# Performance work log

Hardware: AMD Instinct MI355X
Metric: run time of the kernel (lower is better)

The kernel has to match this reference:

```python
import jax, jax.numpy as jnp
import numpy as np

B, T, D, H = 512, 1024, 12, 100


def setup_inputs() -> dict:
    key = jax.random.key(0)
    ks = jax.random.split(key, 5)
    x = jax.random.normal(ks[0], (B, T, D), dtype=jnp.float32)
    Wx = jax.random.normal(ks[1], (D, 4 * H), dtype=jnp.float32) * (1.0 / np.sqrt(D))
    Wh = jax.random.normal(ks[2], (H, 4 * H), dtype=jnp.float32) * (1.0 / np.sqrt(H))
    b = jnp.zeros((4 * H,), dtype=jnp.float32)
    Wd = jax.random.normal(ks[3], (H, D), dtype=jnp.float32) * (1.0 / np.sqrt(H))
    bd = jnp.zeros((D,), dtype=jnp.float32)
    return {"x": x, "Wx": Wx, "Wh": Wh, "b": b, "Wd": Wd, "bd": bd}


def _lstm_seq(x, Wx, Wh, b):
    # Precompute input projection for all timesteps (vectorized GEMM).
    xg = jnp.einsum('btd,dh->bth', x, Wx) + b  # [B, T, 4H]
    xg = jnp.transpose(xg, (1, 0, 2))          # [T, B, 4H] for scan

    def step(carry, xg_t):
        h, c = carry
        z = xg_t + h @ Wh                      # [B, 4H]
        i, f, g, o = jnp.split(z, 4, axis=-1)  # Keras gate order: i, f, c, o
        i = jax.nn.sigmoid(i)
        f = jax.nn.sigmoid(f)
        g = jnp.tanh(g)
        o = jax.nn.sigmoid(o)
        c = f * c + i * g
        h = o * jnp.tanh(c)
        return (h, c), h

    h0 = jnp.zeros((x.shape[0], Wh.shape[0]), dtype=x.dtype)
    c0 = jnp.zeros_like(h0)
    _, hs = jax.lax.scan(step, (h0, c0), xg)   # hs: [T, B, H]
    return jnp.transpose(hs, (1, 0, 2))        # [B, T, H]


def reference(x, Wx, Wh, b, Wd, bd):
    hs = _lstm_seq(x, Wx, Wh, b)               # [B, T, H]
    return jnp.einsum('bth,hd->btd', hs, Wd) + bd  # [B, T, 12]
```

## Files before the change

kernel.cpp:

```cpp
#include <hip/hip_runtime.h>
#include <math.h>

#define T_LEN 1024
#define BATCH 512
#define DIN   12
#define HID   100
#define G4    400
#define MB    4
#define NBLK  (BATCH / MB)
#define AROW  160
#define NW    8
#define NTHR  (NW * 64)
#define CHUNK 64
#define UNROLL 8

typedef _Float16 half8   __attribute__((ext_vector_type(8)));
typedef _Float16 half4_t __attribute__((ext_vector_type(4)));
typedef float    f32x4   __attribute__((ext_vector_type(4)));

static __device__ __forceinline__ float fast_exp2(float v) {
#if __has_builtin(__builtin_amdgcn_exp2f)
    return __builtin_amdgcn_exp2f(v);
#else
    return exp2f(v);
#endif
}
static __device__ __forceinline__ float fast_rcp(float v) {
#if __has_builtin(__builtin_amdgcn_rcpf)
    return __builtin_amdgcn_rcpf(v);
#else
    return 1.0f / v;
#endif
}

__launch_bounds__(NTHR, 2)
__global__ void lstm_mfma_kernel(const float* __restrict__ x,
                                 const float* __restrict__ Wx,
                                 const float* __restrict__ Wh,
                                 const float* __restrict__ b,
                                 const float* __restrict__ Wd,
                                 const float* __restrict__ bd,
                                 float* __restrict__ out) {
    __shared__ __align__(16) char smem[65536];
    const int tid  = threadIdx.x;
    const int wid  = tid >> 6;
    const int lane = tid & 63;
    const int l    = lane & 15;
    const int quad = lane >> 4;
    const int b0   = blockIdx.x * MB;
    const int j    = wid * 16 + l;

    _Float16* stage = (_Float16*)smem;
    half8 bfrag[4][4];
#pragma unroll
    for (int pass = 0; pass < 2; ++pass) {
#pragma unroll
        for (int gg = 0; gg < 2; ++gg) {
            const int G = pass * 2 + gg;
#pragma unroll
            for (int kt = 0; kt < 4; ++kt) {
                half8 v;
#pragma unroll
                for (int jj = 0; jj < 8; ++jj) {
                    const int k = kt * 32 + quad * 8 + jj;
                    float w = 0.f;
                    if (wid < 7) {
                        if (j < HID) {
                            if (k < HID)            w = Wh[k * G4 + G * HID + j];
                            else if (k < HID + DIN) w = Wx[(k - HID) * G4 + G * HID + j];
                        }
                    } else if (G == 0) {
                        if (l < DIN && k < HID)     w = Wd[k * DIN + l];
                    }
                    v[jj] = (_Float16)w;
                }
                *(half8*)&stage[((wid * 8) + (gg * 4 + kt)) * 512 + lane * 8] = v;
            }
        }
        __syncthreads();
#pragma unroll
        for (int gg = 0; gg < 2; ++gg)
#pragma unroll
            for (int kt = 0; kt < 4; ++kt)
                bfrag[pass * 2 + gg][kt] =
                    *(half8*)&stage[((wid * 8) + (gg * 4 + kt)) * 512 + lane * 8];
        __syncthreads();
    }

    f32x4 biasC[4];
#pragma unroll
    for (int G = 0; G < 4; ++G) biasC[G] = (f32x4){0.f, 0.f, 0.f, 0.f};
    if (wid < 7) {
        if (j < HID) {
#pragma unroll
            for (int G = 0; G < 4; ++G) {
                const float bv = b[G * HID + j];
                biasC[G] = (f32x4){bv, bv, bv, bv};
            }
        }
    } else if (l < DIN) {
        const float bv = bd[l];
        biasC[0] = (f32x4){bv, bv, bv, bv};
    }

    _Float16 (*Ah)[MB][AROW] = (_Float16 (*)[MB][AROW])smem;
    _Float16* xchunk = (_Float16*)(smem + 2560);

    auto refill = [&](int c) {
#pragma unroll
        for (int ii = 0; ii < 2; ++ii) {
            const int f = tid + NTHR * ii;
            if (f < (CHUNK * MB * DIN) / 4) {
                const int m  = f / (CHUNK * DIN / 4);
                const int o  = f - m * (CHUNK * DIN / 4);
                const int tt = o / 3;
                const int dd = o - tt * 3;
                const float4 v = *(const float4*)(x +
                    ((size_t)(b0 + m) * T_LEN + c * CHUNK + tt) * DIN + dd * 4);
                half4_t h4;
                h4[0] = (_Float16)v.x; h4[1] = (_Float16)v.y;
                h4[2] = (_Float16)v.z; h4[3] = (_Float16)v.w;
                *(half4_t*)&xchunk[tt * (MB * DIN) + m * DIN + dd * 4] = h4;
            }
        }
    };

    for (int i = tid; i < (2 * MB * AROW) / 2; i += NTHR) ((int*)smem)[i] = 0;
    refill(0);
    __syncthreads();
    if (tid < MB * 3) {
        const int m = tid / 3, part = tid - (tid / 3) * 3;
        *(half4_t*)&Ah[0][m][HID + part * 4] =
            *(const half4_t*)&xchunk[m * DIN + part * 4];
    }
    __syncthreads();

    const bool gate_lane = (wid < 7) && (j < HID);
    const int  arow = l >> 2;
    const float L2E = 1.4426950408889634f;

    float c = 0.f;
    float obuf[UNROLL];

#pragma unroll 1
    for (int tb = 0; tb < T_LEN / UNROLL; ++tb) {
#pragma unroll
        for (int it = 0; it < UNROLL; ++it) {
            const int t  = tb * UNROLL + it;
            const int p  = it & 1;
            const int pn = p ^ 1;

            if (it == UNROLL - 1) {
                if (((tb + 1) & 7) == 0 && (tb + 1) < T_LEN / UNROLL) {
                    refill((tb + 1) >> 3);
                    __syncthreads();
                }
            }

            half8 a[4];
#pragma unroll
            for (int kt = 0; kt < 4; ++kt)
                a[kt] = *(const half8*)&Ah[p][arow][kt * 32 + quad * 8];

            if (wid < 7) {
                f32x4 acc[4];
#pragma unroll
                for (int kt = 0; kt < 4; ++kt)
#pragma unroll
                    for (int G = 0; G < 4; ++G)
                        acc[G] = __builtin_amdgcn_mfma_f32_16x16x32_f16(
                                     a[kt], bfrag[G][kt],
                                     (kt == 0) ? biasC[G] : acc[G], 0, 0, 0);

                if (gate_lane) {
                    const float ei = fast_exp2(-L2E * acc[0][0]);
                    const float ef = fast_exp2(-L2E * acc[1][0]);
                    const float eg = fast_exp2(-2.f * L2E * acc[2][0]);
                    const float eo = fast_exp2(-L2E * acc[3][0]);
                    const float gig = (1.f - eg) * fast_rcp((1.f + ei) * (1.f + eg));
                    const float gf  = fast_rcp(1.f + ef);
                    const float cn  = gf * c + gig;
                    c = cn;
                    const float ec = fast_exp2(-2.f * L2E * cn);
                    const float hv = (1.f - ec) * fast_rcp((1.f + eo) * (1.f + ec));
                    Ah[pn][quad][j] = (_Float16)hv;
                }
            } else {
                f32x4 accP;
#pragma unroll
                for (int kt = 0; kt < 4; ++kt)
                    accP = __builtin_amdgcn_mfma_f32_16x16x32_f16(
                               a[kt], bfrag[0][kt],
                               (kt == 0) ? biasC[0] : accP, 0, 0, 0);
                obuf[it] = accP[0];
                if ((t + 1) < T_LEN && lane < MB * 3) {
                    const int m = lane / 3, part = lane - (lane / 3) * 3;
                    *(half4_t*)&Ah[pn][m][HID + part * 4] =
                        *(const half4_t*)&xchunk[((t + 1) & (CHUNK - 1)) * (MB * DIN)
                                                 + m * DIN + part * 4];
                }
            }
            __syncthreads();
        }
        if (wid == 7 && l < DIN) {
#pragma unroll
            for (int s = 0; s < UNROLL; ++s) {
                const int row = tb * UNROLL + s - 1;
                if (row >= 0)
                    out[((size_t)(b0 + quad) * T_LEN + row) * DIN + l] = obuf[s];
            }
        }
    }

    if (wid == 7) {
        half8 a[4];
#pragma unroll
        for (int kt = 0; kt < 4; ++kt)
            a[kt] = *(const half8*)&Ah[0][arow][kt * 32 + quad * 8];
        f32x4 accP;
#pragma unroll
        for (int kt = 0; kt < 4; ++kt)
            accP = __builtin_amdgcn_mfma_f32_16x16x32_f16(
                       a[kt], bfrag[0][kt],
                       (kt == 0) ? biasC[0] : accP, 0, 0, 0);
        if (l < DIN)
            out[((size_t)(b0 + quad) * T_LEN + (T_LEN - 1)) * DIN + l] = accP[0];
    }
}

extern "C" void kernel_launch(void* const* d_in, const int* in_sizes, int n_in,
                              void* d_out, int out_size, void* d_ws, size_t ws_size,
                              hipStream_t stream) {
    const float* x  = (const float*)d_in[0];
    const float* Wx = (const float*)d_in[1];
    const float* Wh = (const float*)d_in[2];
    const float* b  = (const float*)d_in[3];
    const float* Wd = (const float*)d_in[4];
    const float* bd = (const float*)d_in[5];
    float* out = (float*)d_out;

    lstm_mfma_kernel<<<NBLK, NTHR, 0, stream>>>(x, Wx, Wh, b, Wd, bd, out);
}
```

Baseline: 538.0 us.

## Pack dense output projection into idle lanes of last gate warp; prescale weights

Drops the dedicated eighth wavefront by mapping the 12 output-projection columns onto the unused lanes (j>=100) of the seventh gate warp, whose G=0 fragment now holds Wd. That warp also handles the x staging for the next step. Gate weights and biases are prescaled by -log2(e) (or -2·log2(e) for the cell gate), which removes the per-step multiplies before exp2. The goal is fewer waves per block synchronising at every timestep's barrier and less ALU work on the critical recurrence. The trade-off is that the fp16 weights are stored prescaled, which slightly changes rounding.

```diff
diff --git a/kernel.cpp b/kernel.cpp
--- a/kernel.cpp
+++ b/kernel.cpp
@@ -9,7 +9,7 @@
 #define MB    4
 #define NBLK  (BATCH / MB)
 #define AROW  160
-#define NW    8
+#define NW    7
 #define NTHR  (NW * 64)
 #define CHUNK 64
 #define UNROLL 8
@@ -50,6 +50,8 @@
     const int b0   = blockIdx.x * MB;
     const int j    = wid * 16 + l;
 
+    const float L2E = 1.4426950408889634f;
+
     _Float16* stage = (_Float16*)smem;
     half8 bfrag[4][4];
 #pragma unroll
@@ -57,6 +59,7 @@
 #pragma unroll
         for (int gg = 0; gg < 2; ++gg) {
             const int G = pass * 2 + gg;
+            const float scale = (G == 2) ? (-2.f * L2E) : (-L2E);
 #pragma unroll
             for (int kt = 0; kt < 4; ++kt) {
                 half8 v;
@@ -64,13 +67,11 @@
                 for (int jj = 0; jj < 8; ++jj) {
                     const int k = kt * 32 + quad * 8 + jj;
                     float w = 0.f;
-                    if (wid < 7) {
-                        if (j < HID) {
-                            if (k < HID)            w = Wh[k * G4 + G * HID + j];
-                            else if (k < HID + DIN) w = Wx[(k - HID) * G4 + G * HID + j];
-                        }
+                    if (j < HID) {
+                        if (k < HID)            w = scale * Wh[k * G4 + G * HID + j];
+                        else if (k < HID + DIN) w = scale * Wx[(k - HID) * G4 + G * HID + j];
                     } else if (G == 0) {
-                        if (l < DIN && k < HID)     w = Wd[k * DIN + l];
+                        if (k < HID)            w = Wd[k * DIN + (l - 4)];
                     }
                     v[jj] = (_Float16)w;
                 }
@@ -90,16 +91,15 @@
     f32x4 biasC[4];
 #pragma unroll
     for (int G = 0; G < 4; ++G) biasC[G] = (f32x4){0.f, 0.f, 0.f, 0.f};
-    if (wid < 7) {
-        if (j < HID) {
-#pragma unroll
-            for (int G = 0; G < 4; ++G) {
-                const float bv = b[G * HID + j];
-                biasC[G] = (f32x4){bv, bv, bv, bv};
-            }
-        }
-    } else if (l < DIN) {
-        const float bv = bd[l];
+    if (j < HID) {
+#pragma unroll
+        for (int G = 0; G < 4; ++G) {
+            const float scale = (G == 2) ? (-2.f * L2E) : (-L2E);
+            const float bv = scale * b[G * HID + j];
+            biasC[G] = (f32x4){bv, bv, bv, bv};
+        }
+    } else {
+        const float bv = bd[l - 4];
         biasC[0] = (f32x4){bv, bv, bv, bv};
     }
 
@@ -135,9 +135,8 @@
     }
     __syncthreads();
 
-    const bool gate_lane = (wid < 7) && (j < HID);
+    const bool gate_lane = (j < HID);
     const int  arow = l >> 2;
-    const float L2E = 1.4426950408889634f;
 
     float c = 0.f;
     float obuf[UNROLL];
@@ -162,57 +161,50 @@
             for (int kt = 0; kt < 4; ++kt)
                 a[kt] = *(const half8*)&Ah[p][arow][kt * 32 + quad * 8];
 
-            if (wid < 7) {
-                f32x4 acc[4];
-#pragma unroll
-                for (int kt = 0; kt < 4; ++kt)
-#pragma unroll
-                    for (int G = 0; G < 4; ++G)
-                        acc[G] = __builtin_amdgcn_mfma_f32_16x16x32_f16(
-                                     a[kt], bfrag[G][kt],
-                                     (kt == 0) ? biasC[G] : acc[G], 0, 0, 0);
-
-                if (gate_lane) {
-                    const float ei = fast_exp2(-L2E * acc[0][0]);
-                    const float ef = fast_exp2(-L2E * acc[1][0]);
-                    const float eg = fast_exp2(-2.f * L2E * acc[2][0]);
-                    const float eo = fast_exp2(-L2E * acc[3][0]);
-                    const float gig = (1.f - eg) * fast_rcp((1.f + ei) * (1.f + eg));
-                    const float gf  = fast_rcp(1.f + ef);
-                    const float cn  = gf * c + gig;
-                    c = cn;
-                    const float ec = fast_exp2(-2.f * L2E * cn);
-                    const float hv = (1.f - ec) * fast_rcp((1.f + eo) * (1.f + ec));
-                    Ah[pn][quad][j] = (_Float16)hv;
+            f32x4 acc[4];
+#pragma unroll
+            for (int kt = 0; kt < 4; ++kt)
+#pragma unroll
+                for (int G = 0; G < 4; ++G)
+                    acc[G] = __builtin_amdgcn_mfma_f32_16x16x32_f16(
+                                 a[kt], bfrag[G][kt],
+                                 (kt == 0) ? biasC[G] : acc[G], 0, 0, 0);
+
+            if (gate_lane) {
+                const float ei = fast_exp2(acc[0][0]);
+                const float ef = fast_exp2(acc[1][0]);
+                const float eg = fast_exp2(acc[2][0]);
+                const float eo = fast_exp2(acc[3][0]);
+                const float gig = (1.f - eg) * fast_rcp((1.f + ei) * (1.f + eg));
+                const float gf  = fast_rcp(1.f + ef);
+                const float cn  = gf * c + gig;
+                c = cn;
+                const float ec  = fast_exp2(-2.f * L2E * cn);
+                const float hv  = (1.f - ec) * fast_rcp((1.f + eo) * (1.f + ec));
+                Ah[pn][quad][j] = (_Float16)hv;
+            } else {
+                obuf[it] = acc[0][0];
+                if ((l - 4) < 3 && (t + 1) < T_LEN) {
+                    const int part = l - 4;
+                    *(half4_t*)&Ah[pn][quad][HID + part * 4] =
+                        *(const half4_t*)&xchunk[((t + 1) & (CHUNK - 1)) * (MB * DIN)
+                                                 + quad * DIN + part * 4];
                 }
-            } else {
-                f32x4 accP;
-#pragma unroll
-                for (int kt = 0; kt < 4; ++kt)
-                    accP = __builtin_amdgcn_mfma_f32_16x16x32_f16(
-                               a[kt], bfrag[0][kt],
-                               (kt == 0) ? biasC[0] : accP, 0, 0, 0);
-                obuf[it] = accP[0];
-                if ((t + 1) < T_LEN && lane < MB * 3) {
-                    const int m = lane / 3, part = lane - (lane / 3) * 3;
-                    *(half4_t*)&Ah[pn][m][HID + part * 4] =
-                        *(const half4_t*)&xchunk[((t + 1) & (CHUNK - 1)) * (MB * DIN)
-                                                 + m * DIN + part * 4];
-                }
             }
             __syncthreads();
         }
-        if (wid == 7 && l < DIN) {
+        if (!gate_lane) {
+            const int d = l - 4;
 #pragma unroll
             for (int s = 0; s < UNROLL; ++s) {
                 const int row = tb * UNROLL + s - 1;
                 if (row >= 0)
-                    out[((size_t)(b0 + quad) * T_LEN + row) * DIN + l] = obuf[s];
-            }
-        }
-    }
-
-    if (wid == 7) {
+                    out[((size_t)(b0 + quad) * T_LEN + row) * DIN + d] = obuf[s];
+            }
+        }
+    }
+
+    if (wid == NW - 1) {
         half8 a[4];
 #pragma unroll
         for (int kt = 0; kt < 4; ++kt)
@@ -223,8 +215,8 @@
             accP = __builtin_amdgcn_mfma_f32_16x16x32_f16(
                        a[kt], bfrag[0][kt],
                        (kt == 0) ? biasC[0] : accP, 0, 0, 0);
-        if (l < DIN)
-            out[((size_t)(b0 + quad) * T_LEN + (T_LEN - 1)) * DIN + l] = accP[0];
+        if (l >= 4)
+            out[((size_t)(b0 + quad) * T_LEN + (T_LEN - 1)) * DIN + (l - 4)] = accP[0];
     }
 }
 
```

Result: slower. 554.3 us (+3.0%).
